# Kernel tuning notes

Hardware: AMD Instinct MI355X
Metric: run time of the kernel (lower is better)

## Reference

```python
import jax, jax.numpy as jnp
import numpy as np
from jax import lax

EPS_LN = 1e-5
EPS_NORM = 1e-12


def _layernorm_c(x, w, b):
    # WithBias LayerNorm over channel dim of NCHW (equivalent to to_3d -> LN(-1) -> to_4d)
    mu = jnp.mean(x, axis=1, keepdims=True)
    var = jnp.mean(jnp.square(x - mu), axis=1, keepdims=True)
    return (x - mu) / jnp.sqrt(var + EPS_LN) * w[None, :, None, None] + b[None, :, None, None]


def _conv1x1(x, w):
    # w: [O, C] ; x: [B, C, H, W]
    return jnp.einsum('oc,bchw->bohw', w, x)


def _dwconv3x3(x, w):
    # w: [C, 1, 3, 3], depthwise, padding=1
    C = x.shape[1]
    return lax.conv_general_dilated(
        x, w, window_strides=(1, 1), padding=((1, 1), (1, 1)),
        dimension_numbers=('NCHW', 'OIHW', 'NCHW'), feature_group_count=C)


def setup_inputs() -> dict:
    key = jax.random.key(0)
    ks = jax.random.split(key, 8)
    B, C, H, W = 4, 384, 128, 128
    n_heads = 8
    s = 1.0 / np.sqrt(C)
    inp = {
        'x': jax.random.normal(ks[0], (B, C, H, W), jnp.float32),
        'wq': jax.random.normal(ks[1], (C, C), jnp.float32) * s,
        'wk': jax.random.normal(ks[2], (C, C), jnp.float32) * s,
        'wv': jax.random.normal(ks[3], (C, C), jnp.float32) * s,
        'dwq': jax.random.normal(ks[4], (C, 1, 3, 3), jnp.float32) * (1.0 / 3.0),
        'dwk': jax.random.normal(ks[5], (C, 1, 3, 3), jnp.float32) * (1.0 / 3.0),
        'dwv': jax.random.normal(ks[6], (C, 1, 3, 3), jnp.float32) * (1.0 / 3.0),
        'scale': jnp.ones((n_heads, 1, 1), jnp.float32),
        'ln1_w': jnp.ones((C,), jnp.float32),
        'ln1_b': jnp.zeros((C,), jnp.float32),
        'ln2_w': jnp.ones((C,), jnp.float32),
        'ln2_b': jnp.zeros((C,), jnp.float32),
    }
    return inp


def reference(x, wq, wk, wv, dwq, dwk, dwv, scale, ln1_w, ln1_b, ln2_w, ln2_b):
    B, C, H, W = x.shape
    n_heads = scale.shape[0]
    d = C // n_heads
    L = H * W

    x_norm = _layernorm_c(x, ln1_w, ln1_b)
    q = _dwconv3x3(_conv1x1(x_norm, wq), dwq)
    k = _dwconv3x3(_conv1x1(x_norm, wk), dwk)
    v = _dwconv3x3(_conv1x1(x_norm, wv), dwv)

    # b (n d) h w -> b n d L
    q = q.reshape(B, n_heads, d, L)
    k = k.reshape(B, n_heads, d, L)
    v = v.reshape(B, n_heads, d, L)

    # L2-normalize over spatial dim (F.normalize, eps=1e-12)
    q = q / jnp.maximum(jnp.linalg.norm(q, axis=-1, keepdims=True), EPS_NORM)
    k = k / jnp.maximum(jnp.linalg.norm(k, axis=-1, keepdims=True), EPS_NORM)

    # channel (transposed) attention: [b, n, d, d]
    attn = jnp.einsum('bndl,bnel->bnde', q, k) * scale[None]
    attn = jax.nn.softmax(attn, axis=-1)
    out = jnp.einsum('bnde,bnel->bndl', attn, v)

    out = out.reshape(B, C, H, W)
    return _layernorm_c(out, ln2_w, ln2_b)
```

## Files before the change

kernel.cpp:

```cpp
#include <hip/hip_runtime.h>
#include <hip/hip_bf16.h>
#include <stdint.h>

#define B_ 4
#define C_ 384
#define H_ 128
#define W_ 128
#define L_ (H_*W_)
#define NH 8
#define DH 48
#define SPLIT 8

typedef __attribute__((ext_vector_type(8))) short bf16x8;
typedef __attribute__((ext_vector_type(4))) float f32x4;
typedef unsigned short u16;
typedef unsigned int u32;

__device__ __forceinline__ float bf2f(u16 v){
  union { float f; u32 u; } x; x.u = ((u32)v) << 16; return x.f;
}
__device__ __forceinline__ u16 f2bf(float f){
  __hip_bfloat16 h = __float2bfloat16(f);
  return *reinterpret_cast<u16*>(&h);
}

#define GLOAD_LDS16(g, l) \
  __builtin_amdgcn_global_load_lds((const __attribute__((address_space(1))) u32*)(g), \
                                   (__attribute__((address_space(3))) u32*)(l), 16, 0, 0)

__global__ __launch_bounds__(256) void k_cvt_w(const float* __restrict__ wq,
                                               const float* __restrict__ wk,
                                               const float* __restrict__ wv,
                                               u16* __restrict__ wc){
  int i = blockIdx.x * 256 + threadIdx.x;
  if (i >= 3*C_*C_) return;
  int m = i / C_;
  int c = i - m*C_;
  const float* src = (m < C_) ? wq : (m < 2*C_) ? wk : wv;
  int mm = (m >= 2*C_) ? m - 2*C_ : (m >= C_) ? m - C_ : m;
  wc[i] = f2bf(src[mm*C_ + c]);
}

__global__ __launch_bounds__(256) void k_ln1(const float* __restrict__ x,
                                             const float* __restrict__ w,
                                             const float* __restrict__ b,
                                             u16* __restrict__ xt){
  const int tid = threadIdx.x;
  const int bb = blockIdx.x >> 8;
  const int l0 = (blockIdx.x & 255) << 6;
  const int pg = tid >> 4;
  const int cg = tid & 15;
  const int c0 = cg * 24;
  const float* xp = x + (size_t)bb*C_*L_ + (size_t)c0*L_ + l0 + pg*4;

  f32x4 vals[24];
  #pragma unroll
  for (int ci = 0; ci < 24; ++ci)
    vals[ci] = *reinterpret_cast<const f32x4*>(xp + (size_t)ci*L_);

  f32x4 s = {0.f,0.f,0.f,0.f}, s2 = {0.f,0.f,0.f,0.f};
  #pragma unroll
  for (int ci = 0; ci < 24; ++ci){ s += vals[ci]; s2 += vals[ci]*vals[ci]; }
  #pragma unroll
  for (int m = 1; m < 16; m <<= 1){
    #pragma unroll
    for (int r = 0; r < 4; ++r){
      s[r]  += __shfl_xor(s[r],  m);
      s2[r] += __shfl_xor(s2[r], m);
    }
  }
  f32x4 mu, rstd;
  #pragma unroll
  for (int r = 0; r < 4; ++r){
    mu[r]   = s[r] * (1.f/C_);
    rstd[r] = rsqrtf(s2[r]*(1.f/C_) - mu[r]*mu[r] + 1e-5f);
  }

  u16* dst = xt + ((size_t)bb*L_ + l0 + pg*4)*C_ + c0;
  #pragma unroll
  for (int j = 0; j < 3; ++j){
    f32x4 w0 = *reinterpret_cast<const f32x4*>(w + c0 + j*8);
    f32x4 w1 = *reinterpret_cast<const f32x4*>(w + c0 + j*8 + 4);
    f32x4 b0 = *reinterpret_cast<const f32x4*>(b + c0 + j*8);
    f32x4 b1 = *reinterpret_cast<const f32x4*>(b + c0 + j*8 + 4);
    #pragma unroll
    for (int pp = 0; pp < 4; ++pp){
      uint4 pk;
      u16* tp = reinterpret_cast<u16*>(&pk);
      #pragma unroll
      for (int e = 0; e < 4; ++e)
        tp[e]   = f2bf((vals[j*8+e][pp]   - mu[pp]) * rstd[pp] * w0[e] + b0[e]);
      #pragma unroll
      for (int e = 0; e < 4; ++e)
        tp[4+e] = f2bf((vals[j*8+4+e][pp] - mu[pp]) * rstd[pp] * w1[e] + b1[e]);
      *reinterpret_cast<uint4*>(dst + (size_t)pp*C_ + j*8) = pk;
    }
  }
}

#define SLOTA (128*32)
#define SLOTB (256*32)
__global__ __launch_bounds__(512) void k_gemm(const u16* __restrict__ Wc,
                                              const u16* __restrict__ Xt,
                                              u16* __restrict__ qkv){
  __shared__ u16 As[3*SLOTA];
  __shared__ u16 Bs[3*SLOTB];
  const int tid = threadIdx.x;
  const int wg = (int)blockIdx.x;
  const int lin = (wg & 7) * 288 + (wg >> 3);
  const int bm = lin % 9;
  const int bn = lin / 9;
  const int m0 = bm * 128;
  const int n0 = bn * 256;
  const int w = tid >> 6, lane = tid & 63;
  const int wm = (w >> 2) * 64, wn = (w & 3) * 64;
  const int fr = lane & 15, kqi = lane >> 4;
  const int sslot = kqi ^ ((fr >> 1) & 3);

  f32x4 acc[4][4] = {};

#define STAGE(slot, k0) do { \
    { int rowA_ = tid >> 2, qA_ = tid & 3; \
      int qsA_ = qA_ ^ ((rowA_ >> 1) & 3); \
      GLOAD_LDS16(Wc + (size_t)(m0+rowA_)*384 + (k0) + qsA_*8, As + (slot)*SLOTA + tid*8); } \
    _Pragma("unroll") \
    for (int i_ = 0; i_ < 2; ++i_){ \
      int idx_ = i_*512 + tid; \
      int row_ = idx_ >> 2, q_ = idx_ & 3; \
      int qs_ = q_ ^ ((row_ >> 1) & 3); \
      GLOAD_LDS16(Xt + (size_t)(n0+row_)*384 + (k0) + qs_*8, Bs + (slot)*SLOTB + idx_*8); \
    } } while(0)

  STAGE(0, 0);
  STAGE(1, 32);

  #pragma unroll
  for (int it = 0; it < 12; ++it){
    const int cur = it % 3;
    __builtin_amdgcn_sched_barrier(0);
    if (it < 11) asm volatile("s_waitcnt vmcnt(3)" ::: "memory");
    else         asm volatile("s_waitcnt vmcnt(0)" ::: "memory");
    __builtin_amdgcn_sched_barrier(0);
    __builtin_amdgcn_s_barrier();
    __builtin_amdgcn_sched_barrier(0);
    if (it + 2 < 12) STAGE((it+2)%3, (it+2)*32);

    const u16* Ab = As + cur*SLOTA;
    const u16* Bb = Bs + cur*SLOTB;
    bf16x8 af[4], bfm[4];
    #pragma unroll
    for (int i = 0; i < 4; ++i)
      af[i] = *reinterpret_cast<const bf16x8*>(Ab + (wm + i*16 + fr)*32 + sslot*8);
    #pragma unroll
    for (int j = 0; j < 4; ++j)
      bfm[j] = *reinterpret_cast<const bf16x8*>(Bb + (wn + j*16 + fr)*32 + sslot*8);
    #pragma unroll
    for (int i = 0; i < 4; ++i)
      #pragma unroll
      for (int j = 0; j < 4; ++j)
        acc[i][j] = __builtin_amdgcn_mfma_f32_16x16x32_bf16(af[i], bfm[j], acc[i][j], 0, 0, 0);
  }
#undef STAGE

  #pragma unroll
  for (int i = 0; i < 4; ++i){
    int mbase = m0 + wm + i*16 + (lane >> 4) * 4;
    #pragma unroll
    for (int j = 0; j < 4; ++j){
      int n = n0 + wn + j*16 + fr;
      int bb = n >> 14, l = n & (L_-1);
      #pragma unroll
      for (int r = 0; r < 4; ++r){
        int m = mbase + r;
        int proj = (m >= 2*C_) ? 2 : (m >= C_) ? 1 : 0;
        int c = m - proj*C_;
        qkv[(((size_t)proj*B_ + bb)*C_ + c)*L_ + l] = f2bf(acc[i][j][r]);
      }
    }
  }
}

__global__ __launch_bounds__(256) void k_dwconv(u16* __restrict__ qkv,
                                                const float* __restrict__ dwq,
                                                const float* __restrict__ dwk,
                                                const float* __restrict__ dwv,
                                                float* __restrict__ sumsq){
  __shared__ u16 pl[128*128];
  int pid = blockIdx.x;
  int t = pid / (B_*C_);
  int bc = pid - t*(B_*C_);
  int c = bc % C_;
  const float* dw = ((t == 0) ? dwq : (t == 1) ? dwk : dwv) + c*9;
  u16* plane = qkv + ((size_t)t*B_*C_ + bc) * L_;
  int tid = threadIdx.x;
  #pragma unroll
  for (int i = 0; i < 8; ++i){
    int idx = i*256 + tid;
    *reinterpret_cast<uint4*>(pl + idx*8) = *reinterpret_cast<const uint4*>(plane + idx*8);
  }
  float wgt[9];
  #pragma unroll
  for (int i = 0; i < 9; ++i) wgt[i] = dw[i];
  __syncthreads();

  const int tx = tid & 15;
  const int ty = tid >> 4;
  const int lane = tid & 63;
  const int y0 = ty*8;

  float rv[3][8], rl[3], rr_[3];
  float ss = 0.f;

  #pragma unroll
  for (int i = 0; i < 10; ++i){
    const int sl = i % 3;
    int r = y0 - 1 + i;
    int rc = (r < 0) ? 0 : (r > 127 ? 127 : r);
    uint4 pk = *reinterpret_cast<const uint4*>(pl + rc*128 + tx*8);
    const u16* e = reinterpret_cast<const u16*>(&pk);
    bool oob = (r < 0) || (r > 127);
    #pragma unroll
    for (int k = 0; k < 8; ++k)
      rv[sl][k] = oob ? 0.f : bf2f(e[k]);
    float lft = __shfl(rv[sl][7], lane - 1);
    float rgt = __shfl(rv[sl][0], lane + 1);
    rl[sl]  = (tx == 0)  ? 0.f : lft;
    rr_[sl] = (tx == 15) ? 0.f : rgt;

    if (i >= 2){
      const int sa = (i-2) % 3, sb = (i-1) % 3, sc = i % 3;
      const int y = i - 2;
      float o[8];
      #pragma unroll
      for (int xx = 0; xx < 8; ++xx){
        float am1 = (xx == 0) ? rl[sa]  : rv[sa][xx-1];
        float ap1 = (xx == 7) ? rr_[sa] : rv[sa][xx+1];
        float bm1 = (xx == 0) ? rl[sb]  : rv[sb][xx-1];
        float bp1 = (xx == 7) ? rr_[sb] : rv[sb][xx+1];
        float cm1 = (xx == 0) ? rl[sc]  : rv[sc][xx-1];
        float cp1 = (xx == 7) ? rr_[sc] : rv[sc][xx+1];
        float a = wgt[0]*am1 + wgt[1]*rv[sa][xx] + wgt[2]*ap1
                + wgt[3]*bm1 + wgt[4]*rv[sb][xx] + wgt[5]*bp1
                + wgt[6]*cm1 + wgt[7]*rv[sc][xx] + wgt[8]*cp1;
        o[xx] = a;
        ss += a * a;
      }
      uint4 st;
      u16* sp = reinterpret_cast<u16*>(&st);
      #pragma unroll
      for (int xx = 0; xx < 8; ++xx) sp[xx] = f2bf(o[xx]);
      *reinterpret_cast<uint4*>(plane + (y0 + y)*128 + tx*8) = st;
    }
  }

  if (t < 2){
    #pragma unroll
    for (int off = 32; off > 0; off >>= 1) ss += __shfl_down(ss, off);
    __shared__ float red[4];
    if ((tid & 63) == 0) red[tid >> 6] = ss;
    __syncthreads();
    if (tid == 0) sumsq[t*(B_*C_) + bc] = red[0] + red[1] + red[2] + red[3];
  }
}

__global__ __launch_bounds__(512) void k_qk(const u16* __restrict__ qkv,
                                            float* __restrict__ Spart){
  int gid = blockIdx.x;
  int s = gid / (B_*NH);
  int bn = gid - s*(B_*NH);
  int b = bn / NH, n = bn - b*NH;
  const u16* qb = qkv + ((size_t)b*C_ + n*DH) * L_;
  const u16* kb = qkv + ((size_t)B_*C_ + (size_t)b*C_ + n*DH) * L_;
  int tid = threadIdx.x, w = tid >> 6, lane = tid & 63;
  int fr = lane & 15, kq = (lane >> 4) * 8;
  int l0 = s * (L_/SPLIT) + w * (L_/SPLIT/8);
  f32x4 acc[3][3] = {};
  #pragma unroll
  for (int kk = 0; kk < (L_/SPLIT/8); kk += 32){
    int koff = l0 + kk + kq;
    bf16x8 af[3], bfm[3];
    #pragma unroll
    for (int i = 0; i < 3; ++i) af[i]  = *reinterpret_cast<const bf16x8*>(qb + (size_t)(i*16+fr)*L_ + koff);
    #pragma unroll
    for (int j = 0; j < 3; ++j) bfm[j] = *reinterpret_cast<const bf16x8*>(kb + (size_t)(j*16+fr)*L_ + koff);
    #pragma unroll
    for (int i = 0; i < 3; ++i)
      #pragma unroll
      for (int j = 0; j < 3; ++j)
        acc[i][j] = __builtin_amdgcn_mfma_f32_16x16x32_bf16(af[i], bfm[j], acc[i][j], 0, 0, 0);
  }
  __shared__ float red[8*2304];
  float* rw = red + w*2304;
  #pragma unroll
  for (int i = 0; i < 3; ++i)
    #pragma unroll
    for (int j = 0; j < 3; ++j)
      #pragma unroll
      for (int r = 0; r < 4; ++r){
        int row = i*16 + (lane >> 4)*4 + r;
        int col = j*16 + fr;
        rw[row*48 + col] = acc[i][j][r];
      }
  __syncthreads();
  float* dst = Spart + ((size_t)gid) * 2304;
  for (int idx = tid; idx < 2304; idx += 512){
    float a = 0.f;
    #pragma unroll
    for (int ww = 0; ww < 8; ++ww) a += red[ww*2304 + idx];
    dst[idx] = a;
  }
}

__global__ void k_softmax(const float* __restrict__ Spart,
                          const float* __restrict__ sumsq,
                          const float* __restrict__ scale,
                          u16* __restrict__ attn96){
  int bn = blockIdx.x;
  int b = bn / NH, n = bn - b*NH;
  int i = threadIdx.x;
  if (i >= DH) return;
  const float* sq = sumsq + (size_t)b*C_ + n*DH;
  const float* sk = sumsq + (size_t)B_*C_ + (size_t)b*C_ + n*DH;
  float nq = fmaxf(sqrtf(sq[i]), 1e-12f);
  float sc = scale[n];
  float row[48];
  #pragma unroll
  for (int j = 0; j < DH; ++j){
    float acc = 0.f;
    #pragma unroll
    for (int s = 0; s < SPLIT; ++s)
      acc += Spart[((size_t)(s*(B_*NH) + bn))*2304 + i*48 + j];
    float nk = fmaxf(sqrtf(sk[j]), 1e-12f);
    row[j] = acc / (nq * nk) * sc;
  }
  float m = row[0];
  #pragma unroll
  for (int j = 1; j < DH; ++j) m = fmaxf(m, row[j]);
  float sum = 0.f;
  #pragma unroll
  for (int j = 0; j < DH; ++j){ row[j] = __expf(row[j] - m); sum += row[j]; }
  float inv = 1.f / sum;
  u16* dst = attn96 + ((size_t)bn)*DH*96 + i*96;
  #pragma unroll
  for (int j = 0; j < DH; ++j){
    float a = row[j] * inv;
    u16 hi = f2bf(a);
    float lo = a - bf2f(hi);
    dst[j]      = hi;
    dst[48 + j] = f2bf(lo);
  }
}

#define VT_STRIDE 784
__device__ __forceinline__ int vt_off(int p, int ch){
  return p*VT_STRIDE + ((p>>3)<<4) + 2*ch;
}
__global__ __launch_bounds__(256) void k_av_ln2(const u16* __restrict__ qkv,
                                                const u16* __restrict__ attn96,
                                                const float* __restrict__ w2,
                                                const float* __restrict__ b2,
                                                float* __restrict__ out){
  __shared__ u16 vt[(64*VT_STRIDE + 8*16)/2];
  char* vtb = reinterpret_cast<char*>(vt);
  const int tid = threadIdx.x;
  const int bb = blockIdx.x >> 8;
  const int l0 = (blockIdx.x & 255) << 6;
  const u16* vg = qkv + ((size_t)2*B_*C_ + (size_t)bb*C_)*L_ + l0;

  #pragma unroll
  for (int it = 0; it < 6; ++it){
    int idx = it*256 + tid;
    int cp = idx >> 3, g = idx & 7;
    int c = cp*2;
    uint4 p0 = *reinterpret_cast<const uint4*>(vg + (size_t)c*L_ + g*8);
    uint4 p1 = *reinterpret_cast<const uint4*>(vg + (size_t)(c+1)*L_ + g*8);
    const u16* e0 = reinterpret_cast<const u16*>(&p0);
    const u16* e1 = reinterpret_cast<const u16*>(&p1);
    #pragma unroll
    for (int j = 0; j < 8; ++j){
      int p = g*8 + j;
      u32 packed = ((u32)e0[j]) | (((u32)e1[j]) << 16);
      *reinterpret_cast<u32*>(vtb + vt_off(p, c)) = packed;
    }
  }
  __syncthreads();

  const int w = tid >> 6, lane = tid & 63;
  const int fr = lane & 15, kq = (lane >> 4) * 8;
  const int prow = w*16;
  f32x4 acc[24];
  #pragma unroll
  for (int j = 0; j < 24; ++j) acc[j] = (f32x4){0.f,0.f,0.f,0.f};

  const u16* ab = attn96 + ((size_t)bb*NH)*DH*96;
  #pragma unroll
  for (int n = 0; n < NH; ++n){
    bf16x8 af[3];
    #pragma unroll
    for (int s = 0; s < 3; ++s){
      int ep = s*32 + kq;
      int ch = n*DH + (ep >= 48 ? ep - 48 : ep);
      af[s] = *reinterpret_cast<const bf16x8*>(vtb + vt_off(prow + fr, ch));
    }
    #pragma unroll
    for (int jj = 0; jj < 3; ++jj){
      const u16* arow = ab + ((size_t)n*DH + jj*16 + fr)*96;
      #pragma unroll
      for (int s = 0; s < 3; ++s){
        bf16x8 bf = *reinterpret_cast<const bf16x8*>(arow + s*32 + kq);
        acc[n*3+jj] = __builtin_amdgcn_mfma_f32_16x16x32_bf16(af[s], bf, acc[n*3+jj], 0, 0, 0);
      }
    }
  }

  f32x4 s = {0.f,0.f,0.f,0.f}, s2 = {0.f,0.f,0.f,0.f};
  #pragma unroll
  for (int j = 0; j < 24; ++j){ s += acc[j]; s2 += acc[j]*acc[j]; }
  #pragma unroll
  for (int m = 1; m < 16; m <<= 1){
    #pragma unroll
    for (int r = 0; r < 4; ++r){
      s[r]  += __shfl_xor(s[r],  m);
      s2[r] += __shfl_xor(s2[r], m);
    }
  }
  f32x4 mu, rstd;
  #pragma unroll
  for (int r = 0; r < 4; ++r){
    mu[r]   = s[r] * (1.f/C_);
    rstd[r] = rsqrtf(s2[r]*(1.f/C_) - mu[r]*mu[r] + 1e-5f);
  }
  const int pbase = l0 + prow + (lane>>4)*4;
  #pragma unroll
  for (int j = 0; j < 24; ++j){
    int c = j*16 + fr;
    float wc = w2[c], bc = b2[c];
    f32x4 o;
    #pragma unroll
    for (int r = 0; r < 4; ++r)
      o[r] = (acc[j][r] - mu[r]) * rstd[r] * wc + bc;
    *reinterpret_cast<f32x4*>(out + ((size_t)bb*C_ + c)*L_ + pbase) = o;
  }
}

extern "C" void kernel_launch(void* const* d_in, const int* in_sizes, int n_in,
                              void* d_out, int out_size, void* d_ws, size_t ws_size,
                              hipStream_t stream){
  const float* x     = (const float*)d_in[0];
  const float* wq    = (const float*)d_in[1];
  const float* wk    = (const float*)d_in[2];
  const float* wv    = (const float*)d_in[3];
  const float* dwq   = (const float*)d_in[4];
  const float* dwk   = (const float*)d_in[5];
  const float* dwv   = (const float*)d_in[6];
  const float* scale = (const float*)d_in[7];
  const float* ln1w  = (const float*)d_in[8];
  const float* ln1b  = (const float*)d_in[9];
  const float* ln2w  = (const float*)d_in[10];
  const float* ln2b  = (const float*)d_in[11];
  float* out = (float*)d_out;

  char* ws = (char*)d_ws;
  u16*   qkv    = (u16*)ws;
  u16*   xt     = (u16*)(ws + 150994944);
  u16*   wc     = (u16*)(ws + 201326592);
  float* sumsq  = (float*)(ws + 202211328);
  float* Spart  = (float*)(ws + 202223616);
  u16*   attn96 = (u16*)(ws + 204582912);

  k_cvt_w  <<<1728, 256, 0, stream>>>(wq, wk, wv, wc);
  k_ln1    <<<1024, 256, 0, stream>>>(x, ln1w, ln1b, xt);
  k_gemm   <<<2304, 512, 0, stream>>>(wc, xt, qkv);
  k_dwconv <<<3*B_*C_, 256, 0, stream>>>(qkv, dwq, dwk, dwv, sumsq);
  k_qk     <<<SPLIT*B_*NH, 512, 0, stream>>>(qkv, Spart);
  k_softmax<<<B_*NH, 64, 0, stream>>>(Spart, sumsq, scale, attn96);
  k_av_ln2 <<<1024, 256, 0, stream>>>(qkv, attn96, ln2w, ln2b, out);
}
```

Before: 266.7 us.

## Load GEMM A-tile fragments directly from global into registers, skip LDS

The weight (A) operand of the QKV projection GEMM is no longer staged through shared memory. Each lane now loads its MFMA fragments straight from global memory into registers, prefetching one k-step ahead, and the vmcnt wait counts are retuned to match. This shrinks LDS use to the B buffers only and adds an occupancy hint to launch_bounds, aiming at more resident blocks and fewer LDS reads. The trade-off is redundant global loads of A across warps that share rows, and higher register pressure from the in-flight prefetch.

```diff
diff --git a/kernel.cpp b/kernel.cpp
--- a/kernel.cpp
+++ b/kernel.cpp
@@ -98,12 +98,10 @@
   }
 }
 
-#define SLOTA (128*32)
 #define SLOTB (256*32)
-__global__ __launch_bounds__(512) void k_gemm(const u16* __restrict__ Wc,
-                                              const u16* __restrict__ Xt,
-                                              u16* __restrict__ qkv){
-  __shared__ u16 As[3*SLOTA];
+__global__ __launch_bounds__(512, 4) void k_gemm(const u16* __restrict__ Wc,
+                                                 const u16* __restrict__ Xt,
+                                                 u16* __restrict__ qkv){
   __shared__ u16 Bs[3*SLOTB];
   const int tid = threadIdx.x;
   const int wg = (int)blockIdx.x;
@@ -119,10 +117,12 @@
 
   f32x4 acc[4][4] = {};
 
-#define STAGE(slot, k0) do { \
-    { int rowA_ = tid >> 2, qA_ = tid & 3; \
-      int qsA_ = qA_ ^ ((rowA_ >> 1) & 3); \
-      GLOAD_LDS16(Wc + (size_t)(m0+rowA_)*384 + (k0) + qsA_*8, As + (slot)*SLOTA + tid*8); } \
+  const u16* Arp[4];
+  #pragma unroll
+  for (int i = 0; i < 4; ++i)
+    Arp[i] = Wc + (size_t)(m0 + wm + i*16 + fr)*384 + kqi*8;
+
+#define STAGE_B(slot, k0) do { \
     _Pragma("unroll") \
     for (int i_ = 0; i_ < 2; ++i_){ \
       int idx_ = i_*512 + tid; \
@@ -131,26 +131,30 @@
       GLOAD_LDS16(Xt + (size_t)(n0+row_)*384 + (k0) + qs_*8, Bs + (slot)*SLOTB + idx_*8); \
     } } while(0)
 
-  STAGE(0, 0);
-  STAGE(1, 32);
+  STAGE_B(0, 0);
+  STAGE_B(1, 32);
+  __builtin_amdgcn_sched_barrier(0);
+  bf16x8 af[4];
+  #pragma unroll
+  for (int i = 0; i < 4; ++i)
+    af[i] = *reinterpret_cast<const bf16x8*>(Arp[i]);
+  __builtin_amdgcn_sched_barrier(0);
 
   #pragma unroll
   for (int it = 0; it < 12; ++it){
     const int cur = it % 3;
     __builtin_amdgcn_sched_barrier(0);
-    if (it < 11) asm volatile("s_waitcnt vmcnt(3)" ::: "memory");
-    else         asm volatile("s_waitcnt vmcnt(0)" ::: "memory");
+    if (it == 0)      asm volatile("s_waitcnt vmcnt(6)"  ::: "memory");
+    else if (it < 11) asm volatile("s_waitcnt vmcnt(10)" ::: "memory");
+    else              asm volatile("s_waitcnt vmcnt(8)"  ::: "memory");
     __builtin_amdgcn_sched_barrier(0);
     __builtin_amdgcn_s_barrier();
     __builtin_amdgcn_sched_barrier(0);
-    if (it + 2 < 12) STAGE((it+2)%3, (it+2)*32);
-
-    const u16* Ab = As + cur*SLOTA;
+    if (it + 2 < 12) STAGE_B((it+2)%3, (it+2)*32);
+    __builtin_amdgcn_sched_barrier(0);
+
     const u16* Bb = Bs + cur*SLOTB;
-    bf16x8 af[4], bfm[4];
-    #pragma unroll
-    for (int i = 0; i < 4; ++i)
-      af[i] = *reinterpret_cast<const bf16x8*>(Ab + (wm + i*16 + fr)*32 + sslot*8);
+    bf16x8 bfm[4];
     #pragma unroll
     for (int j = 0; j < 4; ++j)
       bfm[j] = *reinterpret_cast<const bf16x8*>(Bb + (wn + j*16 + fr)*32 + sslot*8);
@@ -159,8 +163,16 @@
       #pragma unroll
       for (int j = 0; j < 4; ++j)
         acc[i][j] = __builtin_amdgcn_mfma_f32_16x16x32_bf16(af[i], bfm[j], acc[i][j], 0, 0, 0);
-  }
-#undef STAGE
+
+    __builtin_amdgcn_sched_barrier(0);
+    if (it + 1 < 12){
+      #pragma unroll
+      for (int i = 0; i < 4; ++i)
+        af[i] = *reinterpret_cast<const bf16x8*>(Arp[i] + (it+1)*32);
+    }
+    __builtin_amdgcn_sched_barrier(0);
+  }
+#undef STAGE_B
 
   #pragma unroll
   for (int i = 0; i < 4; ++i){
```

Measured after the change: 324.0 us. 1.21x slower.
